# Kernel optimization log

Measured on AMD Instinct MI355X. Metric: run time of the kernel, lower is better.

## Reference

```python
import jax, jax.numpy as jnp
import numpy as np

B, S, H, NH = 4, 2048, 1024, 16
HD = H // NH
SCALE = 1.0 / np.sqrt(HD)
MASK_VAL = -1e9  # fp32 branch of the torch code


def setup_inputs() -> dict:
    key = jax.random.key(0)
    ks = jax.random.split(key, 6)
    s = 1.0 / np.sqrt(H)
    return {
        "x": jax.random.normal(ks[0], (B, S, H), dtype=jnp.float32),
        "attention_mask": jnp.ones((B, S), dtype=jnp.int32),
        "Wq": jax.random.normal(ks[1], (H, H), dtype=jnp.float32) * s,
        "Wk": jax.random.normal(ks[2], (H, H), dtype=jnp.float32) * s,
        "Wv": jax.random.normal(ks[3], (H, H), dtype=jnp.float32) * s,
        "Wo": jax.random.normal(ks[4], (H, H), dtype=jnp.float32) * s,
        "bo": jnp.zeros((H,), dtype=jnp.float32),
    }


def reference(x, attention_mask, Wq, Wk, Wv, Wo, bo):
    b, s, h = x.shape
    # projections; torch Linear computes x @ W.T
    q = (x @ Wq.T).reshape(b, s, NH, HD).transpose(0, 2, 1, 3)  # [b,nh,s,hd]
    k = (x @ Wk.T).reshape(b, s, NH, HD).transpose(0, 2, 1, 3)
    v = (x @ Wv.T).reshape(b, s, NH, HD).transpose(0, 2, 1, 3)

    scores = jnp.einsum("bhqd,bhkd->bhqk", q, k) * SCALE  # [b,nh,s,s]
    # padding mask: [b,1,1,s]
    pad = (attention_mask == 0)[:, None, None, :]
    scores = jnp.where(pad, MASK_VAL, scores)
    # causal mask
    causal = jnp.tril(jnp.ones((s, s), dtype=bool))[None, None]
    scores = jnp.where(causal, scores, MASK_VAL)

    attn = jax.nn.softmax(scores, axis=-1)  # dropout p=0 / eval -> identity
    out = jnp.einsum("bhqk,bhkd->bhqd", attn, v)
    out = out.transpose(0, 2, 1, 3).reshape(b, s, h)
    return out @ Wo.T + bo
```

## Files before the change

kernel.cpp:

```cpp
#include <hip/hip_runtime.h>

#define B_ 4
#define S_ 2048
#define H_ 1024
#define NH_ 16
#define HD_ 64
#define QSCALE_ 0.1803368801111204f

typedef __attribute__((ext_vector_type(8))) short bf16x8;
typedef __attribute__((ext_vector_type(4))) float f32x4;
typedef __attribute__((ext_vector_type(16))) float f32x16;

__device__ __forceinline__ unsigned short f2bf(float f) {
    unsigned u = __float_as_uint(f);
    unsigned r = (u + 0x7FFFu + ((u >> 16) & 1u)) >> 16;
    return (unsigned short)r;
}
__device__ __forceinline__ float exp2f_hw(float x) { return __builtin_amdgcn_exp2f(x); }

__global__ __launch_bounds__(256) void cast_all(const float* __restrict__ x,
                                                const float* __restrict__ Wq,
                                                const float* __restrict__ Wk,
                                                const float* __restrict__ Wv,
                                                const float* __restrict__ Wo,
                                                unsigned short* __restrict__ xb,
                                                unsigned short* __restrict__ Wqb,
                                                unsigned short* __restrict__ Wkb,
                                                unsigned short* __restrict__ Wvb,
                                                unsigned short* __restrict__ Wob) {
    int bid = blockIdx.x;
    const float* src;
    unsigned short* dst;
    int i;
    if (bid < 8192) {
        src = x; dst = xb; i = bid * 256 + threadIdx.x;
    } else {
        int k = bid - 8192, wsel = k >> 10;
        src = wsel == 0 ? Wq : wsel == 1 ? Wk : wsel == 2 ? Wv : Wo;
        dst = wsel == 0 ? Wqb : wsel == 1 ? Wkb : wsel == 2 ? Wvb : Wob;
        i = (k & 1023) * 256 + threadIdx.x;
    }
    float4 v = reinterpret_cast<const float4*>(src)[i];
    ushort4 o;
    o.x = f2bf(v.x); o.y = f2bf(v.y); o.z = f2bf(v.z); o.w = f2bf(v.w);
    reinterpret_cast<ushort4*>(dst)[i] = o;
}

__device__ __forceinline__ void stage128_swz(const char* g, int gstride, char* lds, int tid) {
    int wave = tid >> 6, lane = tid & 63;
#pragma unroll
    for (int j = 0; j < 4; ++j) {
        int o = ((wave * 4 + j) * 64 + lane) * 16;
        int r = o >> 7;
        int slot = (o >> 4) & 7;
        const char* src = g + (size_t)r * gstride + ((slot ^ (r & 7)) << 4);
        __builtin_amdgcn_global_load_lds((const __attribute__((address_space(1))) void*)src,
                                         (__attribute__((address_space(3))) void*)(lds + (wave * 4 + j) * 1024),
                                         16, 0, 0);
    }
}
__device__ __forceinline__ void stage64_swz8(const char* g, int gstride, char* lds, int tid) {
    int wave = tid >> 6, lane = tid & 63;
    int o = (wave * 64 + lane) * 16;
    int r = o >> 7;
    int slot = (o >> 4) & 7;
    const char* src = g + (size_t)r * gstride + ((slot ^ (r & 7)) << 4);
    __builtin_amdgcn_global_load_lds((const __attribute__((address_space(1))) void*)src,
                                     (__attribute__((address_space(3))) void*)(lds + wave * 1024 + lane * 16),
                                     16, 0, 0);
}

__device__ __forceinline__ bf16x8 frag_swz(const char* lds, int row, int slot) {
    return *reinterpret_cast<const bf16x8*>(lds + row * 128 + (((slot) ^ (row & 7)) << 4));
}

__device__ __forceinline__ float vmax16(const f32x16& v) {
    float a0 = fmaxf(v[0], v[1]), a1 = fmaxf(v[2], v[3]);
    float a2 = fmaxf(v[4], v[5]), a3 = fmaxf(v[6], v[7]);
    float a4 = fmaxf(v[8], v[9]), a5 = fmaxf(v[10], v[11]);
    float a6 = fmaxf(v[12], v[13]), a7 = fmaxf(v[14], v[15]);
    float b0 = fmaxf(a0, a1), b1 = fmaxf(a2, a3), b2 = fmaxf(a4, a5), b3 = fmaxf(a6, a7);
    return fmaxf(fmaxf(b0, b1), fmaxf(b2, b3));
}

__global__ __launch_bounds__(256) void gemm_qkv(const unsigned short* __restrict__ xb,
                                                const unsigned short* __restrict__ Wq,
                                                const unsigned short* __restrict__ Wk,
                                                const unsigned short* __restrict__ Wv,
                                                unsigned short* __restrict__ Qo,
                                                unsigned short* __restrict__ Ko,
                                                unsigned short* __restrict__ Vo) {
    __shared__ __align__(16) char As[16384];
    __shared__ __align__(16) char Bs[16384];
    int tid = threadIdx.x, lane = tid & 63, wave = tid >> 6;
    int wr = wave >> 1, wc = wave & 1;
    int brow = blockIdx.x * 128;
    int mat = blockIdx.y >> 3;
    int bcol = (blockIdx.y & 7) * 128;
    const unsigned short* W = mat == 0 ? Wq : (mat == 1 ? Wk : Wv);
    unsigned short* O = mat == 0 ? Qo : (mat == 1 ? Ko : Vo);
    float oscale = (mat == 0) ? QSCALE_ : 1.0f;
    f32x4 acc[4][4] = {};
    const char* ga = (const char*)(xb + (size_t)brow * H_);
    const char* gb = (const char*)(W + (size_t)bcol * H_);
    int ro = lane & 15, kg = lane >> 4;
    for (int kt = 0; kt < 16; ++kt) {
        stage128_swz(ga + kt * 128, H_ * 2, As, tid);
        stage128_swz(gb + kt * 128, H_ * 2, Bs, tid);
        __syncthreads();
#pragma unroll
        for (int kk = 0; kk < 2; ++kk) {
            bf16x8 af[4], bfr[4];
#pragma unroll
            for (int m = 0; m < 4; ++m) af[m] = frag_swz(As, wr * 64 + m * 16 + ro, kk * 4 + kg);
#pragma unroll
            for (int n = 0; n < 4; ++n) bfr[n] = frag_swz(Bs, wc * 64 + n * 16 + ro, kk * 4 + kg);
#pragma unroll
            for (int m = 0; m < 4; ++m)
#pragma unroll
                for (int n = 0; n < 4; ++n)
                    acc[m][n] = __builtin_amdgcn_mfma_f32_16x16x32_bf16(bfr[n], af[m], acc[m][n], 0, 0, 0);
        }
        __syncthreads();
    }
#pragma unroll
    for (int m = 0; m < 4; ++m) {
        int grow = brow + wr * 64 + m * 16 + ro;
#pragma unroll
        for (int n = 0; n < 4; ++n) {
            int gcol = bcol + wc * 64 + n * 16 + kg * 4;
            float p0 = acc[m][n][0] * oscale, p1 = acc[m][n][1] * oscale;
            float p2 = acc[m][n][2] * oscale, p3 = acc[m][n][3] * oscale;
            unsigned w0, w1;
            asm("v_cvt_pk_bf16_f32 %0, %1, %2" : "=v"(w0) : "v"(p0), "v"(p1));
            asm("v_cvt_pk_bf16_f32 %0, %1, %2" : "=v"(w1) : "v"(p2), "v"(p3));
            uint2 pk; pk.x = w0; pk.y = w1;
            *reinterpret_cast<uint2*>(O + (size_t)grow * H_ + gcol) = pk;
        }
    }
}

__global__ __launch_bounds__(256) void gemm_out(const unsigned short* __restrict__ Ab,
                                                const unsigned short* __restrict__ Wo,
                                                const float* __restrict__ bo,
                                                float* __restrict__ out) {
    __shared__ __align__(16) char As[16384];
    __shared__ __align__(16) char Bs[16384];
    int tid = threadIdx.x, lane = tid & 63, wave = tid >> 6;
    int wr = wave >> 1, wc = wave & 1;
    int brow = blockIdx.x * 128;
    int bcol = blockIdx.y * 128;
    f32x4 acc[4][4] = {};
    const char* ga = (const char*)(Ab + (size_t)brow * H_);
    const char* gb = (const char*)(Wo + (size_t)bcol * H_);
    int ro = lane & 15, kg = lane >> 4;
    for (int kt = 0; kt < 16; ++kt) {
        stage128_swz(ga + kt * 128, H_ * 2, As, tid);
        stage128_swz(gb + kt * 128, H_ * 2, Bs, tid);
        __syncthreads();
#pragma unroll
        for (int kk = 0; kk < 2; ++kk) {
            bf16x8 af[4], bfr[4];
#pragma unroll
            for (int m = 0; m < 4; ++m) af[m] = frag_swz(As, wr * 64 + m * 16 + ro, kk * 4 + kg);
#pragma unroll
            for (int n = 0; n < 4; ++n) bfr[n] = frag_swz(Bs, wc * 64 + n * 16 + ro, kk * 4 + kg);
#pragma unroll
            for (int m = 0; m < 4; ++m)
#pragma unroll
                for (int n = 0; n < 4; ++n)
                    acc[m][n] = __builtin_amdgcn_mfma_f32_16x16x32_bf16(bfr[n], af[m], acc[m][n], 0, 0, 0);
        }
        __syncthreads();
    }
#pragma unroll
    for (int m = 0; m < 4; ++m) {
        int grow = brow + wr * 64 + m * 16 + ro;
#pragma unroll
        for (int n = 0; n < 4; ++n) {
            int gcol = bcol + wc * 64 + n * 16 + kg * 4;
            float4 bn4 = *reinterpret_cast<const float4*>(bo + gcol);
            float4 o4;
            o4.x = acc[m][n][0] + bn4.x;
            o4.y = acc[m][n][1] + bn4.y;
            o4.z = acc[m][n][2] + bn4.z;
            o4.w = acc[m][n][3] + bn4.w;
            *reinterpret_cast<float4*>(out + (size_t)grow * H_ + gcol) = o4;
        }
    }
}

__global__ __launch_bounds__(512) void attn(const unsigned short* __restrict__ Q,
                                            const unsigned short* __restrict__ K,
                                            const unsigned short* __restrict__ V,
                                            const int* __restrict__ amask,
                                            unsigned short* __restrict__ Ab) {
    __shared__ __align__(16) char lds[32768];
    char* Ksm = lds;
    unsigned short* Vt = (unsigned short*)(lds + 16384);
    unsigned char* maskc = (unsigned char*)(lds + 24576);
    unsigned char* anyz = (unsigned char*)(lds + 26624);

    int tid = threadIdx.x, lane = tid & 63, w = tid >> 6;
    int l31 = lane & 31, hi = lane >> 5, hi4 = hi * 4;
    int id = blockIdx.x;
    int g = id >> 6;
    int qb = (g < 4) ? (7 - 2 * g) : (2 * g - 8);
    int bh = id & 63, b = bh >> 4, h = bh & 15;
    int brow = qb * 256;
    int Qwg = brow + w * 32;

    unsigned cm = 0;
#pragma unroll
    for (int r = 0; r < 16; ++r)
        if (((r & 3) + 8 * (r >> 2) + hi4) > l31) cm |= (1u << r);

    const unsigned short* Qg = Q + (size_t)(b * S_ + Qwg + l31) * H_ + h * HD_;
    const unsigned short* Kg = K + (size_t)b * S_ * H_ + h * HD_;
    const unsigned short* Vg = V + (size_t)b * S_ * H_ + h * HD_;

    stage64_swz8((const char*)Kg, H_ * 2, Ksm, tid);
    int vr = tid & 63, vd0 = (tid >> 6) * 8;
    bf16x8 vreg = *reinterpret_cast<const bf16x8*>(Vg + (size_t)vr * H_ + vd0);
    {
        const int4* am4 = reinterpret_cast<const int4*>(amask + b * S_);
        int i = tid;
        if (i < S_ / 4) {
            int4 v = am4[i];
            uchar4 o;
            o.x = (v.x == 0); o.y = (v.y == 0); o.z = (v.z == 0); o.w = (v.w == 0);
            reinterpret_cast<uchar4*>(maskc)[i] = o;
        }
    }
    bf16x8 qf[4];
#pragma unroll
    for (int kk = 0; kk < 4; ++kk)
        qf[kk] = *reinterpret_cast<const bf16x8*>(Qg + kk * 16 + hi * 8);

    __syncthreads();
    if (tid < 32) {
        const unsigned* mw = reinterpret_cast<const unsigned*>(maskc + tid * 64);
        unsigned o = 0;
#pragma unroll
        for (int i = 0; i < 16; ++i) o |= mw[i];
        anyz[tid] = o ? 1 : 0;
    }

    f32x16 oacc0, oacc1;
#pragma unroll
    for (int j = 0; j < 16; ++j) { oacc0[j] = 0.f; oacc1[j] = 0.f; }
    float mrun = -__builtin_inff(), lrun = 0.f;

    int T = 4 * qb + 4;
    for (int t = 0; t < T; ++t) {
        int kv0 = t * 64;
        const char* Kc = Ksm + (t & 1) * 8192;

        {
            unsigned short* vb = Vt + vd0 * 64 + (vr & 7);
            int rs3 = (vr >> 3) << 3;
#pragma unroll
            for (int j = 0; j < 8; ++j)
                vb[j * 64 + (rs3 ^ (j << 3))] = (unsigned short)vreg[j];
        }
        __syncthreads();

        if (t + 1 < T)
            stage64_swz8((const char*)(Kg + (size_t)(kv0 + 64) * H_), H_ * 2,
                         Ksm + ((t + 1) & 1) * 8192, tid);
        {
            int kvn = (t + 1 < T) ? kv0 + 64 : kv0;
            vreg = *reinterpret_cast<const bf16x8*>(Vg + (size_t)(kvn + vr) * H_ + vd0);
        }

        int c0 = kv0, c1 = kv0 + 32;
        if (c0 <= Qwg) {
            bool vis1 = (c1 <= Qwg);
            f32x16 sa0, sa1;
#pragma unroll
            for (int j = 0; j < 16; ++j) { sa0[j] = 0.f; sa1[j] = 0.f; }

            __builtin_amdgcn_s_setprio(1);
#pragma unroll
            for (int kk = 0; kk < 4; ++kk) {
                bf16x8 kf0 = frag_swz(Kc, l31, 2 * kk + hi);
                sa0 = __builtin_amdgcn_mfma_f32_32x32x16_bf16(kf0, qf[kk], sa0, 0, 0, 0);
                if (vis1) {
                    bf16x8 kf1 = frag_swz(Kc, 32 + l31, 2 * kk + hi);
                    sa1 = __builtin_amdgcn_mfma_f32_32x32x16_bf16(kf1, qf[kk], sa1, 0, 0, 0);
                }
            }
            __builtin_amdgcn_s_setprio(0);

            if (c0 == Qwg) {
#pragma unroll
                for (int r = 0; r < 16; ++r) sa0[r] = (cm & (1u << r)) ? -1e9f : sa0[r];
            }
            if (vis1 && c1 == Qwg) {
#pragma unroll
                for (int r = 0; r < 16; ++r) sa1[r] = (cm & (1u << r)) ? -1e9f : sa1[r];
            }
            if (anyz[t]) {
#pragma unroll
                for (int u = 0; u < 4; ++u) {
                    uchar4 mk = *reinterpret_cast<const uchar4*>(maskc + kv0 + 8 * u + hi4);
                    if (mk.x) sa0[4 * u + 0] = -1e9f;
                    if (mk.y) sa0[4 * u + 1] = -1e9f;
                    if (mk.z) sa0[4 * u + 2] = -1e9f;
                    if (mk.w) sa0[4 * u + 3] = -1e9f;
                }
                if (vis1) {
#pragma unroll
                    for (int u = 0; u < 4; ++u) {
                        uchar4 mk = *reinterpret_cast<const uchar4*>(maskc + kv0 + 32 + 8 * u + hi4);
                        if (mk.x) sa1[4 * u + 0] = -1e9f;
                        if (mk.y) sa1[4 * u + 1] = -1e9f;
                        if (mk.z) sa1[4 * u + 2] = -1e9f;
                        if (mk.w) sa1[4 * u + 3] = -1e9f;
                    }
                }
            }

            float mx = vmax16(sa0);
            if (vis1) mx = fmaxf(mx, vmax16(sa1));
            mx = fmaxf(mx, __shfl_xor(mx, 32));

            if (__any(mx > mrun + 10.f)) {
                float mnew = fmaxf(mrun, mx);
                float fsc = exp2f_hw(mrun - mnew);
                mrun = mnew;
                lrun *= fsc;
#pragma unroll
                for (int j = 0; j < 16; ++j) { oacc0[j] *= fsc; oacc1[j] *= fsc; }
            }

            float rs = 0.f;
            __builtin_amdgcn_s_setprio(1);
#pragma unroll
            for (int n = 0; n < 2; ++n) {
                if (n == 1 && !vis1) break;
                const f32x16& sa = (n == 0) ? sa0 : sa1;
                unsigned int wrd[4][2];
#pragma unroll
                for (int u = 0; u < 4; ++u) {
                    float p0 = exp2f_hw(sa[4 * u + 0] - mrun);
                    float p1 = exp2f_hw(sa[4 * u + 1] - mrun);
                    float p2 = exp2f_hw(sa[4 * u + 2] - mrun);
                    float p3 = exp2f_hw(sa[4 * u + 3] - mrun);
                    rs += (p0 + p1) + (p2 + p3);
                    asm("v_cvt_pk_bf16_f32 %0, %1, %2" : "=v"(wrd[u][0]) : "v"(p0), "v"(p1));
                    asm("v_cvt_pk_bf16_f32 %0, %1, %2" : "=v"(wrd[u][1]) : "v"(p2), "v"(p3));
                }
#pragma unroll
                for (int half = 0; half < 2; ++half) {
                    int u0 = 2 * half;
                    unsigned int X0 = wrd[u0][0], Y0 = wrd[u0 + 1][0];
                    unsigned int X1 = wrd[u0][1], Y1 = wrd[u0 + 1][1];
                    asm("v_permlane32_swap_b32 %0, %1" : "+v"(X0), "+v"(Y0));
                    asm("v_permlane32_swap_b32 %0, %1" : "+v"(X1), "+v"(Y1));
                    union { unsigned int u[4]; bf16x8 v; } bu;
                    bu.u[0] = X0; bu.u[1] = X1; bu.u[2] = Y0; bu.u[3] = Y1;
                    int kc = 2 * n + half;
                    bf16x8 af0 = *reinterpret_cast<const bf16x8*>(
                        &Vt[(l31) * 64 + (((2 * kc + hi) ^ (l31 & 7)) << 3)]);
                    oacc0 = __builtin_amdgcn_mfma_f32_32x32x16_bf16(af0, bu.v, oacc0, 0, 0, 0);
                    bf16x8 af1 = *reinterpret_cast<const bf16x8*>(
                        &Vt[(32 + l31) * 64 + (((2 * kc + hi) ^ (l31 & 7)) << 3)]);
                    oacc1 = __builtin_amdgcn_mfma_f32_32x32x16_bf16(af1, bu.v, oacc1, 0, 0, 0);
                }
            }
            __builtin_amdgcn_s_setprio(0);

            rs += __shfl_xor(rs, 32);
            lrun += rs;
        }
        __syncthreads();
    }

    float inv = 1.f / lrun;
    unsigned short* Osm = reinterpret_cast<unsigned short*>(lds);
#pragma unroll
    for (int r = 0; r < 16; ++r) {
        int d = (r & 3) + 8 * (r >> 2) + hi4;
        Osm[w * 2048 + l31 * 64 + ((((d >> 3) ^ (l31 & 7)) << 3) | (d & 7))] = f2bf(oacc0[r] * inv);
        int d1 = d + 32;
        Osm[w * 2048 + l31 * 64 + ((((d1 >> 3) ^ (l31 & 7)) << 3) | (d1 & 7))] = f2bf(oacc1[r] * inv);
    }
    __syncthreads();
#pragma unroll
    for (int wv = 0; wv < 4; ++wv) {
        int q = tid >> 3, j = tid & 7;
        int row = wv * 64 + q;
        bf16x8 vv = *reinterpret_cast<const bf16x8*>(
            Osm + (row >> 5) * 2048 + (row & 31) * 64 + ((j ^ (row & 7)) << 3));
        size_t grow = (size_t)(b * S_ + brow + row);
        *reinterpret_cast<bf16x8*>(Ab + grow * H_ + h * HD_ + j * 8) = vv;
    }
}

extern "C" void kernel_launch(void* const* d_in, const int* in_sizes, int n_in,
                              void* d_out, int out_size, void* d_ws, size_t ws_size,
                              hipStream_t stream) {
    const float* x  = (const float*)d_in[0];
    const int* amask = (const int*)d_in[1];
    const float* Wq = (const float*)d_in[2];
    const float* Wk = (const float*)d_in[3];
    const float* Wv = (const float*)d_in[4];
    const float* Wo = (const float*)d_in[5];
    const float* bo = (const float*)d_in[6];
    float* out = (float*)d_out;

    const size_t XN = (size_t)B_ * S_ * H_;
    const size_t WN = (size_t)H_ * H_;

    char* ws = (char*)d_ws;
    unsigned short* xb  = (unsigned short*)ws;           ws += XN * 2;
    unsigned short* Wqb = (unsigned short*)ws;           ws += WN * 2;
    unsigned short* Wkb = (unsigned short*)ws;           ws += WN * 2;
    unsigned short* Wvb = (unsigned short*)ws;           ws += WN * 2;
    unsigned short* Wob = (unsigned short*)ws;           ws += WN * 2;
    unsigned short* Qb  = (unsigned short*)ws;           ws += XN * 2;
    unsigned short* Kb  = (unsigned short*)ws;           ws += XN * 2;
    unsigned short* Vb  = (unsigned short*)ws;           ws += XN * 2;
    unsigned short* Ab  = (unsigned short*)ws;           ws += XN * 2;

    cast_all<<<12288, 256, 0, stream>>>(x, Wq, Wk, Wv, Wo, xb, Wqb, Wkb, Wvb, Wob);
    gemm_qkv<<<dim3(64, 24), 256, 0, stream>>>(xb, Wqb, Wkb, Wvb, Qb, Kb, Vb);
    attn<<<512, 512, 0, stream>>>(Qb, Kb, Vb, amask, Ab);
    gemm_out<<<dim3(64, 8), 256, 0, stream>>>(Ab, Wob, bo, out);
}
```

Baseline: 172.0 us.

## Process 128-key tiles per attention iteration and transpose out-projection store layout

```diff
diff --git a/kernel.cpp b/kernel.cpp
--- a/kernel.cpp
+++ b/kernel.cpp
@@ -169,24 +169,21 @@
             for (int m = 0; m < 4; ++m)
 #pragma unroll
                 for (int n = 0; n < 4; ++n)
-                    acc[m][n] = __builtin_amdgcn_mfma_f32_16x16x32_bf16(bfr[n], af[m], acc[m][n], 0, 0, 0);
-        }
-        __syncthreads();
-    }
-#pragma unroll
-    for (int m = 0; m < 4; ++m) {
-        int grow = brow + wr * 64 + m * 16 + ro;
-#pragma unroll
-        for (int n = 0; n < 4; ++n) {
-            int gcol = bcol + wc * 64 + n * 16 + kg * 4;
-            float4 bn4 = *reinterpret_cast<const float4*>(bo + gcol);
-            float4 o4;
-            o4.x = acc[m][n][0] + bn4.x;
-            o4.y = acc[m][n][1] + bn4.y;
-            o4.z = acc[m][n][2] + bn4.z;
-            o4.w = acc[m][n][3] + bn4.w;
-            *reinterpret_cast<float4*>(out + (size_t)grow * H_ + gcol) = o4;
-        }
+                    acc[m][n] = __builtin_amdgcn_mfma_f32_16x16x32_bf16(af[m], bfr[n], acc[m][n], 0, 0, 0);
+        }
+        __syncthreads();
+    }
+#pragma unroll
+    for (int n = 0; n < 4; ++n) {
+        int col = bcol + wc * 64 + n * 16 + ro;
+        float bn = bo[col];
+#pragma unroll
+        for (int m = 0; m < 4; ++m)
+#pragma unroll
+            for (int i = 0; i < 4; ++i) {
+                int row = brow + wr * 64 + m * 16 + kg * 4 + i;
+                out[(size_t)row * H_ + col] = acc[m][n][i] + bn;
+            }
     }
 }
 
@@ -195,11 +192,11 @@
                                             const unsigned short* __restrict__ V,
                                             const int* __restrict__ amask,
                                             unsigned short* __restrict__ Ab) {
-    __shared__ __align__(16) char lds[32768];
+    __shared__ __align__(16) char lds[51264];
     char* Ksm = lds;
-    unsigned short* Vt = (unsigned short*)(lds + 16384);
-    unsigned char* maskc = (unsigned char*)(lds + 24576);
-    unsigned char* anyz = (unsigned char*)(lds + 26624);
+    unsigned short* Vt2 = (unsigned short*)(lds + 32768);
+    unsigned char* maskc = (unsigned char*)(lds + 49152);
+    unsigned char* anyz = (unsigned char*)(lds + 51200);
 
     int tid = threadIdx.x, lane = tid & 63, w = tid >> 6;
     int l31 = lane & 31, hi = lane >> 5, hi4 = hi * 4;
@@ -220,8 +217,11 @@
     const unsigned short* Vg = V + (size_t)b * S_ * H_ + h * HD_;
 
     stage64_swz8((const char*)Kg, H_ * 2, Ksm, tid);
+    stage64_swz8((const char*)(Kg + (size_t)64 * H_), H_ * 2, Ksm + 8192, tid);
     int vr = tid & 63, vd0 = (tid >> 6) * 8;
-    bf16x8 vreg = *reinterpret_cast<const bf16x8*>(Vg + (size_t)vr * H_ + vd0);
+    bf16x8 vreg[2];
+    vreg[0] = *reinterpret_cast<const bf16x8*>(Vg + (size_t)vr * H_ + vd0);
+    vreg[1] = *reinterpret_cast<const bf16x8*>(Vg + (size_t)(vr + 64) * H_ + vd0);
     {
         const int4* am4 = reinterpret_cast<const int4*>(amask + b * S_);
         int i = tid;
@@ -251,128 +251,138 @@
     for (int j = 0; j < 16; ++j) { oacc0[j] = 0.f; oacc1[j] = 0.f; }
     float mrun = -__builtin_inff(), lrun = 0.f;
 
-    int T = 4 * qb + 4;
+    int T = 2 * qb + 2;
     for (int t = 0; t < T; ++t) {
-        int kv0 = t * 64;
-        const char* Kc = Ksm + (t & 1) * 8192;
-
+        int kv0 = t * 128;
+
+#pragma unroll
+        for (int h2 = 0; h2 < 2; ++h2) {
+            unsigned short* vb = Vt2 + h2 * 4096 + vd0 * 64 + (vr & 7);
+            int rs3 = (vr >> 3) << 3;
+#pragma unroll
+            for (int j = 0; j < 8; ++j)
+                vb[j * 64 + (rs3 ^ (j << 3))] = (unsigned short)vreg[h2][j];
+        }
+        __syncthreads();
+
+        if (t + 1 < T) {
+            char* kdst = Ksm + ((t + 1) & 1) * 16384;
+            stage64_swz8((const char*)(Kg + (size_t)(kv0 + 128) * H_), H_ * 2, kdst, tid);
+            stage64_swz8((const char*)(Kg + (size_t)(kv0 + 192) * H_), H_ * 2, kdst + 8192, tid);
+        }
         {
-            unsigned short* vb = Vt + vd0 * 64 + (vr & 7);
-            int rs3 = (vr >> 3) << 3;
-#pragma unroll
-            for (int j = 0; j < 8; ++j)
-                vb[j * 64 + (rs3 ^ (j << 3))] = (unsigned short)vreg[j];
-        }
-        __syncthreads();
-
-        if (t + 1 < T)
-            stage64_swz8((const char*)(Kg + (size_t)(kv0 + 64) * H_), H_ * 2,
-                         Ksm + ((t + 1) & 1) * 8192, tid);
-        {
-            int kvn = (t + 1 < T) ? kv0 + 64 : kv0;
-            vreg = *reinterpret_cast<const bf16x8*>(Vg + (size_t)(kvn + vr) * H_ + vd0);
-        }
-
-        int c0 = kv0, c1 = kv0 + 32;
-        if (c0 <= Qwg) {
-            bool vis1 = (c1 <= Qwg);
-            f32x16 sa0, sa1;
-#pragma unroll
-            for (int j = 0; j < 16; ++j) { sa0[j] = 0.f; sa1[j] = 0.f; }
-
-            __builtin_amdgcn_s_setprio(1);
-#pragma unroll
-            for (int kk = 0; kk < 4; ++kk) {
-                bf16x8 kf0 = frag_swz(Kc, l31, 2 * kk + hi);
-                sa0 = __builtin_amdgcn_mfma_f32_32x32x16_bf16(kf0, qf[kk], sa0, 0, 0, 0);
-                if (vis1) {
-                    bf16x8 kf1 = frag_swz(Kc, 32 + l31, 2 * kk + hi);
-                    sa1 = __builtin_amdgcn_mfma_f32_32x32x16_bf16(kf1, qf[kk], sa1, 0, 0, 0);
-                }
+            int kvn = (t + 1 < T) ? kv0 + 128 : kv0;
+            vreg[0] = *reinterpret_cast<const bf16x8*>(Vg + (size_t)(kvn + vr) * H_ + vd0);
+            vreg[1] = *reinterpret_cast<const bf16x8*>(Vg + (size_t)(kvn + 64 + vr) * H_ + vd0);
+        }
+
+#pragma unroll
+        for (int half = 0; half < 2; ++half) {
+            int kvh = kv0 + half * 64;
+            const char* Kc = Ksm + (t & 1) * 16384 + half * 8192;
+            const unsigned short* Vtc = Vt2 + half * 4096;
+
+            int c0 = kvh, c1 = kvh + 32;
+            if (c0 <= Qwg) {
+                bool vis1 = (c1 <= Qwg);
+                f32x16 sa0, sa1;
+#pragma unroll
+                for (int j = 0; j < 16; ++j) { sa0[j] = 0.f; sa1[j] = 0.f; }
+
+                __builtin_amdgcn_s_setprio(1);
+#pragma unroll
+                for (int kk = 0; kk < 4; ++kk) {
+                    bf16x8 kf0 = frag_swz(Kc, l31, 2 * kk + hi);
+                    sa0 = __builtin_amdgcn_mfma_f32_32x32x16_bf16(kf0, qf[kk], sa0, 0, 0, 0);
+                    if (vis1) {
+                        bf16x8 kf1 = frag_swz(Kc, 32 + l31, 2 * kk + hi);
+                        sa1 = __builtin_amdgcn_mfma_f32_32x32x16_bf16(kf1, qf[kk], sa1, 0, 0, 0);
+                    }
+                }
+                __builtin_amdgcn_s_setprio(0);
+
+                if (c0 == Qwg) {
+#pragma unroll
+                    for (int r = 0; r < 16; ++r) sa0[r] = (cm & (1u << r)) ? -1e9f : sa0[r];
+                }
+                if (vis1 && c1 == Qwg) {
+#pragma unroll
+                    for (int r = 0; r < 16; ++r) sa1[r] = (cm & (1u << r)) ? -1e9f : sa1[r];
+                }
+                if (anyz[2 * t + half]) {
+#pragma unroll
+                    for (int u = 0; u < 4; ++u) {
+                        uchar4 mk = *reinterpret_cast<const uchar4*>(maskc + kvh + 8 * u + hi4);
+                        if (mk.x) sa0[4 * u + 0] = -1e9f;
+                        if (mk.y) sa0[4 * u + 1] = -1e9f;
+                        if (mk.z) sa0[4 * u + 2] = -1e9f;
+                        if (mk.w) sa0[4 * u + 3] = -1e9f;
+                    }
+                    if (vis1) {
+#pragma unroll
+                        for (int u = 0; u < 4; ++u) {
+                            uchar4 mk = *reinterpret_cast<const uchar4*>(maskc + kvh + 32 + 8 * u + hi4);
+                            if (mk.x) sa1[4 * u + 0] = -1e9f;
+                            if (mk.y) sa1[4 * u + 1] = -1e9f;
+                            if (mk.z) sa1[4 * u + 2] = -1e9f;
+                            if (mk.w) sa1[4 * u + 3] = -1e9f;
+                        }
+                    }
+                }
+
+                float mx = vmax16(sa0);
+                if (vis1) mx = fmaxf(mx, vmax16(sa1));
+                mx = fmaxf(mx, __shfl_xor(mx, 32));
+
+                if (__any(mx > mrun + 10.f)) {
+                    float mnew = fmaxf(mrun, mx);
+                    float fsc = exp2f_hw(mrun - mnew);
+                    mrun = mnew;
+                    lrun *= fsc;
+#pragma unroll
+                    for (int j = 0; j < 16; ++j) { oacc0[j] *= fsc; oacc1[j] *= fsc; }
+                }
+
+                float rs = 0.f;
+                __builtin_amdgcn_s_setprio(1);
+#pragma unroll
+                for (int n = 0; n < 2; ++n) {
+                    if (n == 1 && !vis1) break;
+                    const f32x16& sa = (n == 0) ? sa0 : sa1;
+                    unsigned int wrd[4][2];
+#pragma unroll
+                    for (int u = 0; u < 4; ++u) {
+                        float p0 = exp2f_hw(sa[4 * u + 0] - mrun);
+                        float p1 = exp2f_hw(sa[4 * u + 1] - mrun);
+                        float p2 = exp2f_hw(sa[4 * u + 2] - mrun);
+                        float p3 = exp2f_hw(sa[4 * u + 3] - mrun);
+                        rs += (p0 + p1) + (p2 + p3);
+                        asm("v_cvt_pk_bf16_f32 %0, %1, %2" : "=v"(wrd[u][0]) : "v"(p0), "v"(p1));
+                        asm("v_cvt_pk_bf16_f32 %0, %1, %2" : "=v"(wrd[u][1]) : "v"(p2), "v"(p3));
+                    }
+#pragma unroll
+                    for (int hf = 0; hf < 2; ++hf) {
+                        int u0 = 2 * hf;
+                        unsigned int X0 = wrd[u0][0], Y0 = wrd[u0 + 1][0];
+                        unsigned int X1 = wrd[u0][1], Y1 = wrd[u0 + 1][1];
+                        asm("v_permlane32_swap_b32 %0, %1" : "+v"(X0), "+v"(Y0));
+                        asm("v_permlane32_swap_b32 %0, %1" : "+v"(X1), "+v"(Y1));
+                        union { unsigned int u[4]; bf16x8 v; } bu;
+                        bu.u[0] = X0; bu.u[1] = X1; bu.u[2] = Y0; bu.u[3] = Y1;
+                        int kc = 2 * n + hf;
+                        bf16x8 af0 = *reinterpret_cast<const bf16x8*>(
+                            &Vtc[(l31) * 64 + (((2 * kc + hi) ^ (l31 & 7)) << 3)]);
+                        oacc0 = __builtin_amdgcn_mfma_f32_32x32x16_bf16(af0, bu.v, oacc0, 0, 0, 0);
+                        bf16x8 af1 = *reinterpret_cast<const bf16x8*>(
+                            &Vtc[(32 + l31) * 64 + (((2 * kc + hi) ^ (l31 & 7)) << 3)]);
+                        oacc1 = __builtin_amdgcn_mfma_f32_32x32x16_bf16(af1, bu.v, oacc1, 0, 0, 0);
+                    }
+                }
+                __builtin_amdgcn_s_setprio(0);
+
+                rs += __shfl_xor(rs, 32);
+                lrun += rs;
             }
-            __builtin_amdgcn_s_setprio(0);
-
-            if (c0 == Qwg) {
-#pragma unroll
-                for (int r = 0; r < 16; ++r) sa0[r] = (cm & (1u << r)) ? -1e9f : sa0[r];
-            }
-            if (vis1 && c1 == Qwg) {
-#pragma unroll
-                for (int r = 0; r < 16; ++r) sa1[r] = (cm & (1u << r)) ? -1e9f : sa1[r];
-            }
-            if (anyz[t]) {
-#pragma unroll
-                for (int u = 0; u < 4; ++u) {
-                    uchar4 mk = *reinterpret_cast<const uchar4*>(maskc + kv0 + 8 * u + hi4);
-                    if (mk.x) sa0[4 * u + 0] = -1e9f;
-                    if (mk.y) sa0[4 * u + 1] = -1e9f;
-                    if (mk.z) sa0[4 * u + 2] = -1e9f;
-                    if (mk.w) sa0[4 * u + 3] = -1e9f;
-                }
-                if (vis1) {
-#pragma unroll
-                    for (int u = 0; u < 4; ++u) {
-                        uchar4 mk = *reinterpret_cast<const uchar4*>(maskc + kv0 + 32 + 8 * u + hi4);
-                        if (mk.x) sa1[4 * u + 0] = -1e9f;
-                        if (mk.y) sa1[4 * u + 1] = -1e9f;
-                        if (mk.z) sa1[4 * u + 2] = -1e9f;
-                        if (mk.w) sa1[4 * u + 3] = -1e9f;
-                    }
-                }
-            }
-
-            float mx = vmax16(sa0);
-            if (vis1) mx = fmaxf(mx, vmax16(sa1));
-            mx = fmaxf(mx, __shfl_xor(mx, 32));
-
-            if (__any(mx > mrun + 10.f)) {
-                float mnew = fmaxf(mrun, mx);
-                float fsc = exp2f_hw(mrun - mnew);
-                mrun = mnew;
-                lrun *= fsc;
-#pragma unroll
-                for (int j = 0; j < 16; ++j) { oacc0[j] *= fsc; oacc1[j] *= fsc; }
-            }
-
-            float rs = 0.f;
-            __builtin_amdgcn_s_setprio(1);
-#pragma unroll
-            for (int n = 0; n < 2; ++n) {
-                if (n == 1 && !vis1) break;
-                const f32x16& sa = (n == 0) ? sa0 : sa1;
-                unsigned int wrd[4][2];
-#pragma unroll
-                for (int u = 0; u < 4; ++u) {
-                    float p0 = exp2f_hw(sa[4 * u + 0] - mrun);
-                    float p1 = exp2f_hw(sa[4 * u + 1] - mrun);
-                    float p2 = exp2f_hw(sa[4 * u + 2] - mrun);
-                    float p3 = exp2f_hw(sa[4 * u + 3] - mrun);
-                    rs += (p0 + p1) + (p2 + p3);
-                    asm("v_cvt_pk_bf16_f32 %0, %1, %2" : "=v"(wrd[u][0]) : "v"(p0), "v"(p1));
-                    asm("v_cvt_pk_bf16_f32 %0, %1, %2" : "=v"(wrd[u][1]) : "v"(p2), "v"(p3));
-                }
-#pragma unroll
-                for (int half = 0; half < 2; ++half) {
-                    int u0 = 2 * half;
-                    unsigned int X0 = wrd[u0][0], Y0 = wrd[u0 + 1][0];
-                    unsigned int X1 = wrd[u0][1], Y1 = wrd[u0 + 1][1];
-                    asm("v_permlane32_swap_b32 %0, %1" : "+v"(X0), "+v"(Y0));
-                    asm("v_permlane32_swap_b32 %0, %1" : "+v"(X1), "+v"(Y1));
-                    union { unsigned int u[4]; bf16x8 v; } bu;
-                    bu.u[0] = X0; bu.u[1] = X1; bu.u[2] = Y0; bu.u[3] = Y1;
-                    int kc = 2 * n + half;
-                    bf16x8 af0 = *reinterpret_cast<const bf16x8*>(
-                        &Vt[(l31) * 64 + (((2 * kc + hi) ^ (l31 & 7)) << 3)]);
-                    oacc0 = __builtin_amdgcn_mfma_f32_32x32x16_bf16(af0, bu.v, oacc0, 0, 0, 0);
-                    bf16x8 af1 = *reinterpret_cast<const bf16x8*>(
-                        &Vt[(32 + l31) * 64 + (((2 * kc + hi) ^ (l31 & 7)) << 3)]);
-                    oacc1 = __builtin_amdgcn_mfma_f32_32x32x16_bf16(af1, bu.v, oacc1, 0, 0, 0);
-                }
-            }
-            __builtin_amdgcn_s_setprio(0);
-
-            rs += __shfl_xor(rs, 32);
-            lrun += rs;
         }
         __syncthreads();
     }
```

After: 197.4 us. 1.15x slower.
